# Optimization experiments

Hardware: AMD Instinct MI355X
Metric: run time of the kernel (lower is better)

Reference implementation:

```python
import jax, jax.numpy as jnp
import numpy as np

HEADS = 8
DIM_HEAD = 64
SCALE = DIM_HEAD ** -0.5

def layernorm_ch(x, g, eps=1e-5):
    # channel-wise LayerNorm over dim=1 (NCHW), biased variance
    mean = jnp.mean(x, axis=1, keepdims=True)
    var = jnp.var(x, axis=1, keepdims=True)
    return (x - mean) * jax.lax.rsqrt(var + eps) * g[None, :, None, None]

def setup_inputs() -> dict:
    key = jax.random.key(0)
    ks = jax.random.split(key, 4)
    B, C, H, W = 16, 512, 64, 64
    hidden = HEADS * DIM_HEAD
    x = jax.random.normal(ks[0], (B, C, H, W), dtype=jnp.float32)
    w_qkv = jax.random.normal(ks[1], (3 * hidden, C), dtype=jnp.float32) * (C ** -0.5)
    w_out = jax.random.normal(ks[2], (C, hidden), dtype=jnp.float32) * (hidden ** -0.5)
    b_out = jnp.zeros((C,), dtype=jnp.float32)
    g_out = jnp.ones((C,), dtype=jnp.float32)
    g_ln = jnp.ones((C,), dtype=jnp.float32)
    return {"x": x, "w_qkv": w_qkv, "w_out": w_out, "b_out": b_out, "g_out": g_out, "g_ln": g_ln}

def reference(x, w_qkv, w_out, b_out, g_out, g_ln):
    B, C, H, W = x.shape
    n = H * W
    x_norm = layernorm_ch(x, g_ln)
    # 1x1 conv == channel GEMM: [B,3*hidden,H,W]
    qkv = jnp.einsum('oc,bchw->bohw', w_qkv, x_norm)
    q, k, v = jnp.split(qkv, 3, axis=1)
    # b (h d) x y -> b h d n
    def to_heads(t):
        return t.reshape(B, HEADS, DIM_HEAD, n)
    q, k, v = to_heads(q), to_heads(k), to_heads(v)
    q = jax.nn.softmax(q, axis=-2) * SCALE   # softmax over d
    k = jax.nn.softmax(k, axis=-1)           # softmax over n
    v = v / n
    context = jnp.einsum('bhdn,bhen->bhde', k, v)
    out = jnp.einsum('bhde,bhdn->bhen', context, q)
    out = out.reshape(B, HEADS * DIM_HEAD, H, W)
    out = jnp.einsum('oc,bchw->bohw', w_out, out) + b_out[None, :, None, None]
    out = layernorm_ch(out, g_out)
    return out + x
```

## Files before the change

### kernel.cpp

```cpp
#include <hip/hip_runtime.h>
#include <math.h>

#define CCH    512
#define HWN    4096
#define NPIX   65536
#define OC3    1536
#define QSCALE 0.125f
#define LN_EPS 1e-5f

typedef _Float16 h16;
typedef h16  f16x8 __attribute__((ext_vector_type(8)));
typedef float f32x4 __attribute__((ext_vector_type(4)));

__device__ __forceinline__ float waveReduceSum(float v) {
#pragma unroll
    for (int off = 32; off; off >>= 1) v += __shfl_xor(v, off);
    return v;
}

__device__ __forceinline__ void gl_lds16(const void* g, void* l) {
    __builtin_amdgcn_global_load_lds((const __attribute__((address_space(1))) void*)g,
                                     (__attribute__((address_space(3))) void*)l, 16, 0, 0);
}

__global__ __launch_bounds__(64) void prep_w(const float* __restrict__ w_qkv,
                                             const float* __restrict__ g_ln,
                                             const float* __restrict__ w_out,
                                             h16* __restrict__ wg_h,
                                             float* __restrict__ s,
                                             h16* __restrict__ wo_h) {
    const int o = blockIdx.x, lane = threadIdx.x;
    if (o < OC3) {
        float sum = 0.f;
#pragma unroll
        for (int j = 0; j < 8; ++j) {
            const int c = lane + j * 64;
            const float w = w_qkv[(size_t)o * CCH + c] * g_ln[c];
            wg_h[(size_t)o * CCH + c] = (h16)(w * 64.f);
            sum += w;
        }
        sum = waveReduceSum(sum);
        if (lane == 0) s[o] = sum;
    } else {
        const int r = o - OC3;
#pragma unroll
        for (int j = 0; j < 8; ++j) {
            const int c = lane + j * 64;
            wo_h[(size_t)r * CCH + c] = (h16)(w_out[(size_t)r * CCH + c] * 64.f);
        }
    }
}

__global__ __launch_bounds__(256) void transpose_cvt(const float* __restrict__ src,
                                                     h16* __restrict__ dhi,
                                                     float* __restrict__ psum,
                                                     float* __restrict__ psq) {
    __shared__ float tile[64][65];
    __shared__ float ps1[4][64], ps2[4][64];
    const int b = blockIdx.z, c0 = blockIdx.y * 64, p0 = blockIdx.x * 64;
    const int t = threadIdx.x;
    const float* sb = src + ((size_t)b * CCH + c0) * HWN + p0;
    const int rc = t >> 4, cc4 = (t & 15) * 4;
#pragma unroll
    for (int ps = 0; ps < 4; ++ps) {
        const float4 v = *(const float4*)(sb + (size_t)(rc + ps * 16) * HWN + cc4);
        tile[rc + ps * 16][cc4 + 0] = v.x;
        tile[rc + ps * 16][cc4 + 1] = v.y;
        tile[rc + ps * 16][cc4 + 2] = v.z;
        tile[rc + ps * 16][cc4 + 3] = v.w;
    }
    __syncthreads();
    {
        const int q = t >> 6, px = t & 63;
        float s1 = 0.f, s2 = 0.f;
#pragma unroll
        for (int c = q * 16; c < q * 16 + 16; ++c) {
            const float v = tile[c][px];
            s1 += v; s2 += v * v;
        }
        ps1[q][px] = s1; ps2[q][px] = s2;
    }
    const int pr0 = t >> 3, cs = (t & 7) * 8;
#pragma unroll
    for (int ps = 0; ps < 2; ++ps) {
        const int pr = pr0 + ps * 32;
        f16x8 vh;
#pragma unroll
        for (int q = 0; q < 8; ++q) vh[q] = (h16)tile[cs + q][pr];
        const size_t o = ((size_t)b * HWN + p0 + pr) * CCH + c0 + cs;
        *(f16x8*)(dhi + o) = vh;
    }
    __syncthreads();
    if (t < 64) {
        const float s1 = ps1[0][t] + ps1[1][t] + ps1[2][t] + ps1[3][t];
        const float s2 = ps2[0][t] + ps2[1][t] + ps2[2][t] + ps2[3][t];
        const size_t gp = (size_t)b * HWN + p0 + t;
        psum[(size_t)(c0 >> 6) * NPIX + gp] = s1;
        psq [(size_t)(c0 >> 6) * NPIX + gp] = s2;
    }
}

__global__ __launch_bounds__(256) void qkv_gemm(const h16* __restrict__ Ahg,
                                                const h16* __restrict__ Bhg,
                                                const float* __restrict__ sv,
                                                const float* __restrict__ psum,
                                                const float* __restrict__ psq,
                                                h16* __restrict__ qout) {
    __shared__ __align__(16) h16 Ah[8192], Bh[8192];
    __shared__ float mnS[128], rsS[128];
    const int tid = threadIdx.x;
    const int om = blockIdx.x * 128;
    const int by0 = blockIdx.y;
    const int by  = (by0 & 7) * 64 + (by0 >> 3);
    const int p0  = by * 128;

    const int srow = tid >> 2;
    const int skh  = ((tid & 3) ^ (srow & 3)) * 8;
    const size_t a0 = (size_t)(om + srow) * CCH + skh;
    const size_t b0 = (size_t)(p0 + srow) * CCH + skh;
    const int wofs = (tid >> 6) * 512;

    const int lane = tid & 63;
    const int wv = tid >> 6;
    const int wm = (wv >> 1) * 64, wn = (wv & 1) * 64;
    const int lr = lane & 15, kg = lane >> 4;
    const int swz = (kg ^ (lr & 3)) * 8;

    f32x4 acc[4][4];
#pragma unroll
    for (int i = 0; i < 4; ++i)
#pragma unroll
        for (int j = 0; j < 4; ++j) acc[i][j] = {0.f, 0.f, 0.f, 0.f};

#define STAGE(KC)                                                     \
    do {                                                              \
        gl_lds16(Ahg + a0 + (KC), Ah + wofs);                         \
        gl_lds16(Ahg + a0 + (KC) + 64 * CCH, Ah + 2048 + wofs);       \
        gl_lds16(Ahg + a0 + (KC) + 32, Ah + 4096 + wofs);             \
        gl_lds16(Ahg + a0 + (KC) + 32 + 64 * CCH, Ah + 6144 + wofs);  \
        gl_lds16(Bhg + b0 + (KC), Bh + wofs);                         \
        gl_lds16(Bhg + b0 + (KC) + 64 * CCH, Bh + 2048 + wofs);       \
        gl_lds16(Bhg + b0 + (KC) + 32, Bh + 4096 + wofs);             \
        gl_lds16(Bhg + b0 + (KC) + 32 + 64 * CCH, Bh + 6144 + wofs);  \
    } while (0)

    STAGE(0);
    if (tid < 128) {
        const int gp = p0 + tid;
        float s1 = 0.f, s2 = 0.f;
#pragma unroll
        for (int cb = 0; cb < 8; ++cb) {
            s1 += psum[(size_t)cb * NPIX + gp];
            s2 += psq [(size_t)cb * NPIX + gp];
        }
        const float m = s1 * (1.f / 512.f);
        float var = s2 * (1.f / 512.f) - m * m;
        var = fmaxf(var, 0.f);
        mnS[tid] = m;
        rsS[tid] = rsqrtf(var + LN_EPS);
    }

#pragma unroll 1
    for (int kc = 0; kc < 512; kc += 64) {
        __syncthreads();
        f16x8 ah[2][4], bh[2][4];
#pragma unroll
        for (int ks = 0; ks < 2; ++ks)
#pragma unroll
            for (int i = 0; i < 4; ++i) {
                const int ra = ks * 4096 + (wm + i * 16 + lr) * 32 + swz;
                ah[ks][i] = *(const f16x8*)(Ah + ra);
                const int rb = ks * 4096 + (wn + i * 16 + lr) * 32 + swz;
                bh[ks][i] = *(const f16x8*)(Bh + rb);
            }
        __syncthreads();
        if (kc + 64 < 512) STAGE(kc + 64);
#pragma unroll
        for (int ks = 0; ks < 2; ++ks)
#pragma unroll
            for (int i = 0; i < 4; ++i)
#pragma unroll
                for (int j = 0; j < 4; ++j)
                    acc[i][j] = __builtin_amdgcn_mfma_f32_16x16x32_f16(ah[ks][i], bh[ks][j], acc[i][j], 0, 0, 0);
    }
#undef STAGE

    const int b = p0 >> 12, hw0 = p0 & 4095;
    float mn[4], rs[4];
#pragma unroll
    for (int j = 0; j < 4; ++j) {
        const int px = wn + j * 16 + lr;
        mn[j] = mnS[px]; rs[j] = rsS[px];
    }
#pragma unroll
    for (int i = 0; i < 4; ++i)
#pragma unroll
        for (int r = 0; r < 4; ++r) {
            const int o = om + wm + i * 16 + kg * 4 + r;
            const float so = sv[o];
            h16* dst = qout + ((size_t)b * OC3 + o) * HWN;
#pragma unroll
            for (int j = 0; j < 4; ++j) {
                const int hw = hw0 + wn + j * 16 + lr;
                dst[hw] = (h16)(rs[j] * (acc[i][j][r] * (1.f / 64.f) - mn[j] * so));
            }
        }
}

__global__ __launch_bounds__(256) void ctx_partial(const h16* __restrict__ qkv16,
                                                   float* __restrict__ ctp) {
    __shared__ float kt[64][68];
    __shared__ float vt[64][68];

    const int bh = blockIdx.y, ci = blockIdx.x;
    const int b = bh >> 3, h = bh & 7;
    const h16* kb = qkv16 + ((size_t)b * OC3 + CCH  + h * 64) * HWN;
    const h16* vb = qkv16 + ((size_t)b * OC3 + 1024 + h * 64) * HWN;
    const int tid = threadIdx.x;

    const int d  = tid >> 2;
    const int td = tid & 15, te = tid >> 4;

    float mx = -1e30f;
    for (int t = 0; t < 8; ++t) {
        const int n0 = ci * 512 + t * 64;
#pragma unroll
        for (int jj = 0; jj < 2; ++jj) {
            const int nn = (tid & 3) * 8 + jj * 32;
            const f16x8 kv = *(const f16x8*)(kb + (size_t)d * HWN + n0 + nn);
#pragma unroll
            for (int u = 0; u < 8; ++u) mx = fmaxf(mx, (float)kv[u]);
        }
    }
    mx = fmaxf(mx, __shfl_xor(mx, 1));
    mx = fmaxf(mx, __shfl_xor(mx, 2));

    float zt = 0.f;
    float acc[4][4];
#pragma unroll
    for (int i = 0; i < 4; ++i)
#pragma unroll
        for (int j = 0; j < 4; ++j) acc[i][j] = 0.f;

    for (int t = 0; t < 8; ++t) {
        const int n0 = ci * 512 + t * 64;
        __syncthreads();
#pragma unroll
        for (int jj = 0; jj < 2; ++jj) {
            const int nn = (tid & 3) * 8 + jj * 32;
            const f16x8 kv = *(const f16x8*)(kb + (size_t)d * HWN + n0 + nn);
            const f16x8 vv = *(const f16x8*)(vb + (size_t)d * HWN + n0 + nn);
#pragma unroll
            for (int u = 0; u < 8; ++u) {
                const float e = __expf((float)kv[u] - mx);
                zt += e;
                kt[nn + u][d] = e;
                vt[nn + u][d] = (float)vv[u];
            }
        }
        __syncthreads();
#pragma unroll
        for (int nn = 0; nn < 64; ++nn) {
            float kf[4], vf[4];
            *(float4*)kf = *(const float4*)&kt[nn][td * 4];
            *(float4*)vf = *(const float4*)&vt[nn][te * 4];
#pragma unroll
            for (int i = 0; i < 4; ++i)
#pragma unroll
                for (int j = 0; j < 4; ++j)
                    acc[i][j] = fmaf(kf[i], vf[j], acc[i][j]);
        }
    }
    zt += __shfl_xor(zt, 1);
    zt += __shfl_xor(zt, 2);

    float* dst = ctp + ((size_t)bh * 8 + ci) * 4224;
#pragma unroll
    for (int i = 0; i < 4; ++i) {
        const float4 o4 = make_float4(acc[i][0], acc[i][1], acc[i][2], acc[i][3]);
        *(float4*)(dst + (td * 4 + i) * 64 + te * 4) = o4;
    }
    if ((tid & 3) == 0) {
        dst[4096 + d] = zt;
        dst[4160 + d] = mx;
    }
}

__global__ __launch_bounds__(256) void ctx_reduce(const float* __restrict__ ctp,
                                                  float* __restrict__ ct) {
    __shared__ float w[8][64];
    __shared__ float rz[64];
    const int bh = blockIdx.x;
    const int tid = threadIdx.x;
    const float* src = ctp + (size_t)bh * 8 * 4224;
    if (tid < 64) {
        float M = -1e30f;
#pragma unroll
        for (int ci = 0; ci < 8; ++ci)
            M = fmaxf(M, src[(size_t)ci * 4224 + 4160 + tid]);
        float Z = 0.f;
#pragma unroll
        for (int ci = 0; ci < 8; ++ci) {
            const float ww = __expf(src[(size_t)ci * 4224 + 4160 + tid] - M);
            w[ci][tid] = ww;
            Z += ww * src[(size_t)ci * 4224 + 4096 + tid];
        }
        rz[tid] = 1.f / Z;
    }
    __syncthreads();
    float* dst = ct + (size_t)bh * 4096;
    for (int e4 = tid * 4; e4 < 4096; e4 += 1024) {
        const int d = e4 >> 6;
        float4 sum = make_float4(0.f, 0.f, 0.f, 0.f);
#pragma unroll
        for (int ci = 0; ci < 8; ++ci) {
            const float4 v = *(const float4*)(src + (size_t)ci * 4224 + e4);
            const float ww = w[ci][d];
            sum.x += ww * v.x; sum.y += ww * v.y;
            sum.z += ww * v.z; sum.w += ww * v.w;
        }
        const float r = rz[d];
        sum.x *= r; sum.y *= r; sum.z *= r; sum.w *= r;
        *(float4*)(dst + e4) = sum;
    }
}

__global__ __launch_bounds__(256) void attn_out(const h16* __restrict__ qkv16,
                                                const float* __restrict__ ct,
                                                h16* __restrict__ at) {
    __shared__ float cts[64][68];
    __shared__ float qt[64][68];

    const int bh = blockIdx.y, ci = blockIdx.x;
    const int b = bh >> 3, h = bh & 7;
    const h16* qb = qkv16 + ((size_t)b * OC3 + h * 64) * HWN;
    const int tid = threadIdx.x;

    for (int i4 = tid * 4; i4 < 4096; i4 += 1024) {
        const float4 v = *(const float4*)(ct + (size_t)bh * 4096 + i4);
        *(float4*)&cts[i4 >> 6][i4 & 63] = v;
    }

    const int d  = tid >> 2;
    const int te = tid & 15, tn = tid >> 4;
    const int rn = tid >> 2, d0q = (tid & 3) * 16;

    for (int t = 0; t < 8; ++t) {
        const int n0 = ci * 512 + t * 64;
        __syncthreads();
#pragma unroll
        for (int jj = 0; jj < 2; ++jj) {
            const int nn = (tid & 3) * 8 + jj * 32;
            const f16x8 qv = *(const f16x8*)(qb + (size_t)d * HWN + n0 + nn);
#pragma unroll
            for (int u = 0; u < 8; ++u) qt[nn + u][d] = (float)qv[u];
        }
        __syncthreads();
        {
            float mx = -1e30f;
#pragma unroll
            for (int dd = 0; dd < 16; ++dd) mx = fmaxf(mx, qt[rn][d0q + dd]);
            mx = fmaxf(mx, __shfl_xor(mx, 1));
            mx = fmaxf(mx, __shfl_xor(mx, 2));
            float sm = 0.f;
#pragma unroll
            for (int dd = 0; dd < 16; ++dd) sm += __expf(qt[rn][d0q + dd] - mx);
            sm += __shfl_xor(sm, 1);
            sm += __shfl_xor(sm, 2);
            const float sc = 512.f * QSCALE / sm;
#pragma unroll
            for (int dd = 0; dd < 16; ++dd)
                qt[rn][d0q + dd] = __expf(qt[rn][d0q + dd] - mx) * sc;
        }
        __syncthreads();
        float acc[4][4];
#pragma unroll
        for (int i = 0; i < 4; ++i)
#pragma unroll
            for (int j = 0; j < 4; ++j) acc[i][j] = 0.f;
#pragma unroll
        for (int dd = 0; dd < 64; ++dd) {
            float cv[4];
            *(float4*)cv = *(const float4*)&cts[dd][te * 4];
            const float q0 = qt[tn * 4 + 0][dd];
            const float q1 = qt[tn * 4 + 1][dd];
            const float q2 = qt[tn * 4 + 2][dd];
            const float q3 = qt[tn * 4 + 3][dd];
#pragma unroll
            for (int i = 0; i < 4; ++i) {
                acc[i][0] = fmaf(cv[i], q0, acc[i][0]);
                acc[i][1] = fmaf(cv[i], q1, acc[i][1]);
                acc[i][2] = fmaf(cv[i], q2, acc[i][2]);
                acc[i][3] = fmaf(cv[i], q3, acc[i][3]);
            }
        }
        __syncthreads();
#pragma unroll
        for (int i = 0; i < 4; ++i)
#pragma unroll
            for (int j = 0; j < 4; ++j)
                qt[tn * 4 + j][te * 4 + i] = acc[i][j];
        __syncthreads();
        {
            const int px = tid >> 2, e0 = (tid & 3) * 16;
            f16x8 vh0, vh1;
#pragma unroll
            for (int u = 0; u < 8; ++u) {
                vh0[u] = (h16)qt[px][e0 + u];
                vh1[u] = (h16)qt[px][e0 + 8 + u];
            }
            const size_t o = ((size_t)b * HWN + n0 + px) * CCH + h * 64 + e0;
            *(f16x8*)(at + o)     = vh0;
            *(f16x8*)(at + o + 8) = vh1;
        }
    }
}

__global__ __launch_bounds__(512) void out_fused(const h16* __restrict__ wo_hi,
                                                 const h16* __restrict__ at,
                                                 const float* __restrict__ b_out,
                                                 const float* __restrict__ g_out,
                                                 const float* __restrict__ x,
                                                 float* __restrict__ out) {
    __shared__ __align__(16) h16 Alds[512 * 32];
    __shared__ __align__(16) h16 Blds[128 * 32];
    __shared__ float red1[4][128], red2[4][128];
    __shared__ float mnS[128], rsS[128];

    const int tid = threadIdx.x;
    const int p0 = blockIdx.x * 128;
    const int b = p0 >> 12, hw0 = p0 & 4095;

    const int trow = tid >> 2;
    const int skh  = ((tid & 3) ^ (trow & 3)) * 8;
    const size_t aoff = (size_t)trow * CCH + skh;
    const size_t boff = (size_t)p0 * CCH + aoff;
    const int wofs = (tid >> 6) * 512;

    const int wv = tid >> 6;
    const int wm = (wv >> 1) * 128, wn = (wv & 1) * 64;
    const int lane = tid & 63;
    const int lr = lane & 15, kg = lane >> 4;
    const int swz = (kg ^ (lr & 3)) * 8;

    f32x4 acc[8][4];
#pragma unroll
    for (int i = 0; i < 8; ++i)
#pragma unroll
        for (int j = 0; j < 4; ++j) acc[i][j] = {0.f, 0.f, 0.f, 0.f};

#define STAGEF(S)                                                           \
    do {                                                                    \
        const int kc_ = (S) * 32;                                           \
        gl_lds16(wo_hi + aoff + kc_,               Alds + wofs);            \
        gl_lds16(wo_hi + aoff + kc_ + 128 * CCH,   Alds + 4096 + wofs);     \
        gl_lds16(wo_hi + aoff + kc_ + 256 * CCH,   Alds + 8192 + wofs);     \
        gl_lds16(wo_hi + aoff + kc_ + 384 * CCH,   Alds + 12288 + wofs);    \
        gl_lds16(at + boff + kc_,                  Blds + wofs);            \
    } while (0)

    STAGEF(0);
#pragma unroll 1
    for (int s = 0; s < 16; ++s) {
        __syncthreads();
        f16x8 af[8], bf[4];
#pragma unroll
        for (int i = 0; i < 8; ++i)
            af[i] = *(const f16x8*)(Alds + (wm + i * 16 + lr) * 32 + swz);
#pragma unroll
        for (int j = 0; j < 4; ++j)
            bf[j] = *(const f16x8*)(Blds + (wn + j * 16 + lr) * 32 + swz);
        __syncthreads();
        if (s < 15) STAGEF(s + 1);
#pragma unroll
        for (int i = 0; i < 8; ++i)
#pragma unroll
            for (int j = 0; j < 4; ++j)
                acc[i][j] = __builtin_amdgcn_mfma_f32_16x16x32_f16(af[i], bf[j], acc[i][j], 0, 0, 0);
    }
#undef STAGEF

#pragma unroll
    for (int i = 0; i < 8; ++i) {
        const int o = wm + i * 16 + kg * 4;
        const float4 bb = *(const float4*)(b_out + o);
#pragma unroll
        for (int j = 0; j < 4; ++j) {
            acc[i][j][0] = acc[i][j][0] * (1.f / 134217728.f) + bb.x;
            acc[i][j][1] = acc[i][j][1] * (1.f / 134217728.f) + bb.y;
            acc[i][j][2] = acc[i][j][2] * (1.f / 134217728.f) + bb.z;
            acc[i][j][3] = acc[i][j][3] * (1.f / 134217728.f) + bb.w;
        }
    }
    float s1[4], s2[4];
#pragma unroll
    for (int j = 0; j < 4; ++j) {
        s1[j] = 0.f; s2[j] = 0.f;
#pragma unroll
        for (int i = 0; i < 8; ++i)
#pragma unroll
            for (int r = 0; r < 4; ++r) {
                const float v = acc[i][j][r];
                s1[j] += v; s2[j] += v * v;
            }
        s1[j] += __shfl_xor(s1[j], 16); s1[j] += __shfl_xor(s1[j], 32);
        s2[j] += __shfl_xor(s2[j], 16); s2[j] += __shfl_xor(s2[j], 32);
    }
    if (kg == 0) {
#pragma unroll
        for (int j = 0; j < 4; ++j) {
            red1[wv >> 1][wn + j * 16 + lr] = s1[j];
            red2[wv >> 1][wn + j * 16 + lr] = s2[j];
        }
    }
    __syncthreads();
    if (tid < 128) {
        const float S1 = red1[0][tid] + red1[1][tid] + red1[2][tid] + red1[3][tid];
        const float S2 = red2[0][tid] + red2[1][tid] + red2[2][tid] + red2[3][tid];
        const float m = S1 * (1.f / 512.f);
        float var = S2 * (1.f / 512.f) - m * m;
        var = fmaxf(var, 0.f);
        mnS[tid] = m;
        rsS[tid] = rsqrtf(var + LN_EPS);
    }
    __syncthreads();
    float mj[4], rj[4];
#pragma unroll
    for (int j = 0; j < 4; ++j) {
        const int px = wn + j * 16 + lr;
        mj[j] = mnS[px]; rj[j] = rsS[px];
    }
#pragma unroll
    for (int i = 0; i < 8; ++i) {
        const int o = wm + i * 16 + kg * 4;
        const float4 gg = *(const float4*)(g_out + o);
#pragma unroll
        for (int r = 0; r < 4; ++r) {
            const float g = (r == 0) ? gg.x : (r == 1) ? gg.y : (r == 2) ? gg.z : gg.w;
            const float* xr = x + ((size_t)b * CCH + o + r) * HWN + hw0 + wn;
            float* dr = out + ((size_t)b * CCH + o + r) * HWN + hw0 + wn;
#pragma unroll
            for (int j = 0; j < 4; ++j) {
                const int c = j * 16 + lr;
                dr[c] = (acc[i][j][r] - mj[j]) * rj[j] * g + xr[c];
            }
        }
    }
}

extern "C" void kernel_launch(void* const* d_in, const int* in_sizes, int n_in,
                              void* d_out, int out_size, void* d_ws, size_t ws_size,
                              hipStream_t stream) {
    (void)in_sizes; (void)n_in; (void)out_size;
    const float* x     = (const float*)d_in[0];
    const float* w_qkv = (const float*)d_in[1];
    const float* w_out = (const float*)d_in[2];
    const float* b_out = (const float*)d_in[3];
    const float* g_out = (const float*)d_in[4];
    const float* g_ln  = (const float*)d_in[5];
    float* out = (float*)d_out;
    float* ws  = (float*)d_ws;

    float* s    = ws;
    float* ct   = s + OC3;
    float* ctp  = ct + 524288;
    float* psum = ctp;
    float* psq  = psum + 524288;
    h16*  wg_hi = (h16*)(ctp + 4325376);
    h16*  wo_hi = wg_hi + 786432;
    h16*  qkv16 = wo_hi + 262144;
    h16*  at    = qkv16 + 100663296;
    h16*  xt_hi = (h16*)d_out;

    const size_t need = 72484352ULL * 4ULL;
    if (ws_size < need) return;

    prep_w       <<<2048, 64, 0, stream>>>(w_qkv, g_ln, w_out, wg_hi, s, wo_hi);
    transpose_cvt<<<dim3(64, 8, 16), 256, 0, stream>>>(x, xt_hi, psum, psq);
    qkv_gemm     <<<dim3(12, 512), 256, 0, stream>>>(wg_hi, xt_hi,
                                                     s, psum, psq, qkv16);
    ctx_partial  <<<dim3(8, 128), 256, 0, stream>>>(qkv16, ctp);
    ctx_reduce   <<<128, 256, 0, stream>>>(ctp, ct);
    attn_out     <<<dim3(8, 128), 256, 0, stream>>>(qkv16, ct, at);
    out_fused    <<<512, 512, 0, stream>>>(wo_hi, at,
                                           b_out, g_out, x, out);
}
```

Baseline: 460.9 us.

## Enlarge QKV GEMM tile to 128x256 with 512 threads and split k-step loads

The QKV GEMM block tile grows from 128x128 to 128x256 pixels, with 8 waves per block and half as many blocks. Each A (weight) tile is now reused across twice as many pixels, which cuts global and LDS traffic per output. The inner loop also issues the first k-half MFMAs before loading the second half's fragments, which shortens register live ranges and overlaps LDS reads with compute. In exchange, LDS use per block rises, occupancy may drop, and the grid has fewer blocks.

```diff
diff --git a/kernel.cpp b/kernel.cpp
--- a/kernel.cpp
+++ b/kernel.cpp
@@ -100,29 +100,29 @@
     }
 }
 
-__global__ __launch_bounds__(256) void qkv_gemm(const h16* __restrict__ Ahg,
+__global__ __launch_bounds__(512) void qkv_gemm(const h16* __restrict__ Ahg,
                                                 const h16* __restrict__ Bhg,
                                                 const float* __restrict__ sv,
                                                 const float* __restrict__ psum,
                                                 const float* __restrict__ psq,
                                                 h16* __restrict__ qout) {
-    __shared__ __align__(16) h16 Ah[8192], Bh[8192];
-    __shared__ float mnS[128], rsS[128];
+    __shared__ __align__(16) h16 Ah[8192];
+    __shared__ __align__(16) h16 Bh[16384];
+    __shared__ float mnS[256], rsS[256];
     const int tid = threadIdx.x;
     const int om = blockIdx.x * 128;
     const int by0 = blockIdx.y;
-    const int by  = (by0 & 7) * 64 + (by0 >> 3);
-    const int p0  = by * 128;
+    const int by  = (by0 & 7) * 32 + (by0 >> 3);
+    const int p0  = by * 256;
 
     const int srow = tid >> 2;
     const int skh  = ((tid & 3) ^ (srow & 3)) * 8;
     const size_t a0 = (size_t)(om + srow) * CCH + skh;
     const size_t b0 = (size_t)(p0 + srow) * CCH + skh;
-    const int wofs = (tid >> 6) * 512;
 
     const int lane = tid & 63;
     const int wv = tid >> 6;
-    const int wm = (wv >> 1) * 64, wn = (wv & 1) * 64;
+    const int wm = (wv >> 2) * 64, wn = (wv & 3) * 64;
     const int lr = lane & 15, kg = lane >> 4;
     const int swz = (kg ^ (lr & 3)) * 8;
 
@@ -132,20 +132,18 @@
 #pragma unroll
         for (int j = 0; j < 4; ++j) acc[i][j] = {0.f, 0.f, 0.f, 0.f};
 
-#define STAGE(KC)                                                     \
-    do {                                                              \
-        gl_lds16(Ahg + a0 + (KC), Ah + wofs);                         \
-        gl_lds16(Ahg + a0 + (KC) + 64 * CCH, Ah + 2048 + wofs);       \
-        gl_lds16(Ahg + a0 + (KC) + 32, Ah + 4096 + wofs);             \
-        gl_lds16(Ahg + a0 + (KC) + 32 + 64 * CCH, Ah + 6144 + wofs);  \
-        gl_lds16(Bhg + b0 + (KC), Bh + wofs);                         \
-        gl_lds16(Bhg + b0 + (KC) + 64 * CCH, Bh + 2048 + wofs);       \
-        gl_lds16(Bhg + b0 + (KC) + 32, Bh + 4096 + wofs);             \
-        gl_lds16(Bhg + b0 + (KC) + 32 + 64 * CCH, Bh + 6144 + wofs);  \
+#define STAGE(KC)                                                          \
+    do {                                                                   \
+        gl_lds16(Ahg + a0 + (KC),                 Ah + tid * 8);           \
+        gl_lds16(Ahg + a0 + (KC) + 32,            Ah + 4096 + tid * 8);    \
+        gl_lds16(Bhg + b0 + (KC),                 Bh + tid * 8);           \
+        gl_lds16(Bhg + b0 + (KC) + 128 * CCH,     Bh + 4096 + tid * 8);    \
+        gl_lds16(Bhg + b0 + (KC) + 32,            Bh + 8192 + tid * 8);    \
+        gl_lds16(Bhg + b0 + (KC) + 32 + 128 * CCH, Bh + 12288 + tid * 8);  \
     } while (0)
 
     STAGE(0);
-    if (tid < 128) {
+    if (tid < 256) {
         const int gp = p0 + tid;
         float s1 = 0.f, s2 = 0.f;
 #pragma unroll
@@ -163,25 +161,29 @@
 #pragma unroll 1
     for (int kc = 0; kc < 512; kc += 64) {
         __syncthreads();
-        f16x8 ah[2][4], bh[2][4];
-#pragma unroll
-        for (int ks = 0; ks < 2; ++ks)
-#pragma unroll
-            for (int i = 0; i < 4; ++i) {
-                const int ra = ks * 4096 + (wm + i * 16 + lr) * 32 + swz;
-                ah[ks][i] = *(const f16x8*)(Ah + ra);
-                const int rb = ks * 4096 + (wn + i * 16 + lr) * 32 + swz;
-                bh[ks][i] = *(const f16x8*)(Bh + rb);
-            }
+        f16x8 a0f[4], b0f[4], a1f[4], b1f[4];
+#pragma unroll
+        for (int i = 0; i < 4; ++i) {
+            a0f[i] = *(const f16x8*)(Ah + (wm + i * 16 + lr) * 32 + swz);
+            b0f[i] = *(const f16x8*)(Bh + (wn + i * 16 + lr) * 32 + swz);
+        }
+#pragma unroll
+        for (int i = 0; i < 4; ++i)
+#pragma unroll
+            for (int j = 0; j < 4; ++j)
+                acc[i][j] = __builtin_amdgcn_mfma_f32_16x16x32_f16(a0f[i], b0f[j], acc[i][j], 0, 0, 0);
+#pragma unroll
+        for (int i = 0; i < 4; ++i) {
+            a1f[i] = *(const f16x8*)(Ah + 4096 + (wm + i * 16 + lr) * 32 + swz);
+            b1f[i] = *(const f16x8*)(Bh + 8192 + (wn + i * 16 + lr) * 32 + swz);
+        }
         __syncthreads();
         if (kc + 64 < 512) STAGE(kc + 64);
 #pragma unroll
-        for (int ks = 0; ks < 2; ++ks)
-#pragma unroll
-            for (int i = 0; i < 4; ++i)
-#pragma unroll
-                for (int j = 0; j < 4; ++j)
-                    acc[i][j] = __builtin_amdgcn_mfma_f32_16x16x32_f16(ah[ks][i], bh[ks][j], acc[i][j], 0, 0, 0);
+        for (int i = 0; i < 4; ++i)
+#pragma unroll
+            for (int j = 0; j < 4; ++j)
+                acc[i][j] = __builtin_amdgcn_mfma_f32_16x16x32_f16(a1f[i], b1f[j], acc[i][j], 0, 0, 0);
     }
 #undef STAGE
 
@@ -577,7 +579,7 @@
 
     prep_w       <<<2048, 64, 0, stream>>>(w_qkv, g_ln, w_out, wg_hi, s, wo_hi);
     transpose_cvt<<<dim3(64, 8, 16), 256, 0, stream>>>(x, xt_hi, psum, psq);
-    qkv_gemm     <<<dim3(12, 512), 256, 0, stream>>>(wg_hi, xt_hi,
+    qkv_gemm     <<<dim3(12, 256), 512, 0, stream>>>(wg_hi, xt_hi,
                                                      s, psum, psq, qkv16);
     ctx_partial  <<<dim3(8, 128), 256, 0, stream>>>(qkv16, ctp);
     ctx_reduce   <<<128, 256, 0, stream>>>(ctp, ct);
```

Result: no change. 452.5 us (-1.8%).
